# Performance work log

Measured on AMD Instinct MI355X. Metric: run time of the kernel, lower is better.

The kernel has to match this reference:

```python
import jax, jax.numpy as jnp
import numpy as np
import math

B, T, C = 1, 2048, 2048
N_HEAD = 32
N_QUERY_GROUPS = 8
HEAD_SIZE = 64
ROPE_N_ELEM = 16  # int(0.25 * 64)
Q_PER_KV = N_HEAD // N_QUERY_GROUPS  # 4
QKV_DIM = (N_HEAD + 2 * N_QUERY_GROUPS) * HEAD_SIZE  # 3072


def setup_inputs() -> dict:
    key = jax.random.key(0)
    ks = jax.random.split(key, 7)
    x = jax.random.normal(ks[0], (B, T, C), dtype=jnp.float32)
    # realistic rope tables
    inv_freq = 1.0 / (10000.0 ** (jnp.arange(0, ROPE_N_ELEM, 2, dtype=jnp.float32) / ROPE_N_ELEM))
    t = jnp.arange(T, dtype=jnp.float32)
    freqs = jnp.outer(t, inv_freq)                       # [T, rope/2]
    emb = jnp.concatenate([freqs, freqs], axis=-1)       # [T, rope]
    cos, sin = jnp.cos(emb), jnp.sin(emb)
    s = 0.02
    W_attn = jax.random.normal(ks[1], (QKV_DIM, C), dtype=jnp.float32) * s
    b_attn = jax.random.normal(ks[2], (QKV_DIM,), dtype=jnp.float32) * s
    W_proj = jax.random.normal(ks[3], (C, N_HEAD * HEAD_SIZE), dtype=jnp.float32) * s
    b_proj = jax.random.normal(ks[4], (C,), dtype=jnp.float32) * s
    return {"x": x, "cos": cos, "sin": sin, "W_attn": W_attn, "b_attn": b_attn,
            "W_proj": W_proj, "b_proj": b_proj}


def _apply_rope(t, cos, sin):
    # t: [B, H, T, rope]; cos/sin: [T, rope]
    half = t.shape[-1] // 2
    t1, t2 = t[..., :half], t[..., half:]
    rotated = jnp.concatenate([-t2, t1], axis=-1)
    return t * cos + rotated * sin


def reference(x, cos, sin, W_attn, b_attn, W_proj, b_proj):
    Bc, Tc, Cc = x.shape
    qkv = x @ W_attn.T + b_attn                                   # [B, T, 3072]
    qkv = qkv.reshape(Bc, Tc, N_QUERY_GROUPS, Q_PER_KV + 2, HEAD_SIZE)
    qkv = qkv.transpose(0, 2, 3, 1, 4)                            # [B, G, q_per_kv+2, T, hs]
    q = qkv[:, :, :Q_PER_KV]                                      # [B, G, q_per_kv, T, hs]
    k = qkv[:, :, Q_PER_KV:Q_PER_KV + 1]                          # [B, G, 1, T, hs]
    v = qkv[:, :, Q_PER_KV + 1:]
    # GQA expand (n_query_groups != n_head, prefill path)
    k = jnp.broadcast_to(k, (Bc, N_QUERY_GROUPS, Q_PER_KV, Tc, HEAD_SIZE))
    v = jnp.broadcast_to(v, (Bc, N_QUERY_GROUPS, Q_PER_KV, Tc, HEAD_SIZE))
    q = q.reshape(Bc, N_HEAD, Tc, HEAD_SIZE)
    k = k.reshape(Bc, N_HEAD, Tc, HEAD_SIZE)
    v = v.reshape(Bc, N_HEAD, Tc, HEAD_SIZE)
    # partial RoPE on first ROPE_N_ELEM dims
    q = jnp.concatenate([_apply_rope(q[..., :ROPE_N_ELEM], cos, sin), q[..., ROPE_N_ELEM:]], axis=-1)
    k = jnp.concatenate([_apply_rope(k[..., :ROPE_N_ELEM], cos, sin), k[..., ROPE_N_ELEM:]], axis=-1)
    # causal SDPA with scale 1/sqrt(head_size)
    scale = 1.0 / math.sqrt(HEAD_SIZE)
    scores = jnp.einsum('bhqd,bhkd->bhqk', q, k) * scale          # [B, H, T, T]
    causal = jnp.tril(jnp.ones((Tc, Tc), dtype=bool))
    scores = jnp.where(causal, scores, jnp.finfo(scores.dtype).min)
    attn = jax.nn.softmax(scores, axis=-1)
    y = jnp.einsum('bhqk,bhkd->bhqd', attn, v)                    # [B, H, T, hs]
    y = y.transpose(0, 2, 1, 3).reshape(Bc, Tc, N_HEAD * HEAD_SIZE)
    return y @ W_proj.T + b_proj
```

## Files before the change

kernel.cpp:

```cpp
#include <hip/hip_runtime.h>
#include <hip/hip_bf16.h>

using u16 = unsigned short;
typedef float f32x4 __attribute__((ext_vector_type(4)));
typedef __bf16 bf16x8 __attribute__((ext_vector_type(8)));

#define T_SEQ 2048
#define C_DIM 2048
#define QKV_DIM 3072
#define N_HEAD 32
#define N_GROUPS 8
#define HEAD_SIZE 64
#define ROPE_N 16
#define NEG_BIG (-1e30f)
#define LS 72

__device__ inline float bf2f(u16 u) {
    union { float f; unsigned v; } x; x.v = ((unsigned)u) << 16; return x.f;
}
__device__ inline u16 f2bf(float f) {
    __bf16 h = (__bf16)f;
    return *(u16*)&h;
}

__device__ __forceinline__ void gl_lds16(const u16* g, u16* l) {
    __builtin_amdgcn_global_load_lds(
        (const __attribute__((address_space(1))) unsigned int*)g,
        (__attribute__((address_space(3))) unsigned int*)l,
        16, 0, 0);
}

__global__ void detect_dtype(const u16* __restrict__ x, int* __restrict__ flag)
{
    __shared__ int s[256];
    int cnt = 0;
    for (int i = threadIdx.x; i < 8192; i += 256) {
        int e = (x[i] >> 7) & 0xFF;
        cnt += (e >= 0xC0);
    }
    s[threadIdx.x] = cnt;
    __syncthreads();
    if (threadIdx.x == 0) {
        int tot = 0;
        for (int i = 0; i < 256; i++) tot += s[i];
        flag[0] = (tot > 64) ? 1 : 0;
    }
}

struct ConvDesc {
    const void* src[7];
    u16*        dst[7];
    int         off8[8];
};

__global__ void convert_all(ConvDesc cd, const int* __restrict__ flag)
{
    int gid = blockIdx.x * blockDim.x + threadIdx.x;
    if (gid >= cd.off8[7]) return;
    int seg = 0;
#pragma unroll
    for (int s = 1; s < 7; s++) seg += (gid >= cd.off8[s]);
    int i = (gid - cd.off8[seg]) * 8;
    if (*flag) {
        const float4* s = (const float4*)((const float*)cd.src[seg] + i);
        float4 a = s[0], b = s[1];
        __attribute__((aligned(16))) u16 o[8] = {
            f2bf(a.x), f2bf(a.y), f2bf(a.z), f2bf(a.w),
            f2bf(b.x), f2bf(b.y), f2bf(b.z), f2bf(b.w) };
        *(int4*)(cd.dst[seg] + i) = *(const int4*)o;
    } else {
        *(int4*)(cd.dst[seg] + i) = *(const int4*)((const u16*)cd.src[seg] + i);
    }
}

__global__ __launch_bounds__(256) void gemm_qkv_rope(
    const u16* __restrict__ A, const u16* __restrict__ W,
    const u16* __restrict__ bias,
    const u16* __restrict__ ccos, const u16* __restrict__ csin,
    u16* __restrict__ Qout, u16* __restrict__ Kout, u16* __restrict__ Vtout)
{
    __shared__ __attribute__((aligned(16))) u16 lds_a[64 * 32];
    __shared__ __attribute__((aligned(16))) u16 lds_b[128 * 32];

    const int tid  = threadIdx.x;
    const int wave = tid >> 6;
    const int lane = tid & 63;
    const int quad = lane >> 4;
    const int l16  = lane & 15;
    const int bm = blockIdx.y * 64;
    const int bn = blockIdx.x * 128;
    const int K = C_DIM;

    f32x4 acc[4][2] = {};

    const int ra = tid >> 2,          ca = (tid & 3) * 8;
    const int rb0 = tid >> 2,         cb0 = (tid & 3) * 8;
    const int rb1 = (tid + 256) >> 2, cb1 = (tid & 3) * 8;

    for (int k0 = 0; k0 < K; k0 += 32) {
        __syncthreads();
        gl_lds16(A + (size_t)(bm + ra) * K + k0 + ca,  lds_a + tid * 8);
        gl_lds16(W + (size_t)(bn + rb0) * K + k0 + cb0, lds_b + tid * 8);
        gl_lds16(W + (size_t)(bn + rb1) * K + k0 + cb1, lds_b + (tid + 256) * 8);
        __syncthreads();

        bf16x8 afr[4], bfr[2];
#pragma unroll
        for (int i = 0; i < 4; i++)
            afr[i] = *(const bf16x8*)(lds_a + (i * 16 + l16) * 32 + quad * 8);
#pragma unroll
        for (int j = 0; j < 2; j++)
            bfr[j] = *(const bf16x8*)(lds_b + (wave * 32 + j * 16 + l16) * 32 + quad * 8);
#pragma unroll
        for (int i = 0; i < 4; i++)
#pragma unroll
            for (int j = 0; j < 2; j++)
                acc[i][j] = __builtin_amdgcn_mfma_f32_16x16x32_bf16(afr[i], bfr[j], acc[i][j], 0, 0, 0);
    }

#pragma unroll
    for (int j = 0; j < 2; j++) {
        const int colb = bn + wave * 32 + j * 16;
        const int col  = colb + l16;
        const int slot = (colb % 384) >> 6;
        const int g    = colb / 384;
        const int dbase = colb & 63;
        const int d    = dbase + l16;
        const float bv = bf2f(bias[col]);
        const bool rope = (dbase == 0) && (slot != 5);
#pragma unroll
        for (int i = 0; i < 4; i++) {
            const int trow = bm + i * 16 + quad * 4;
#pragma unroll
            for (int r = 0; r < 4; r++) {
                float v = acc[i][j][r] + bv;
                float outv = v;
                if (rope) {
                    float part = __shfl_xor(v, 8, 64);
                    float rot = (l16 < 8) ? -part : part;
                    float cc = bf2f(ccos[(trow + r) * ROPE_N + l16]);
                    float ss = bf2f(csin[(trow + r) * ROPE_N + l16]);
                    outv = v * cc + rot * ss;
                }
                const int t = trow + r;
                if (slot < 4) {
                    int hh = g * 4 + slot;
                    Qout[((size_t)hh * T_SEQ + t) * 64 + d] = f2bf(outv * 0.125f);
                } else if (slot == 4) {
                    Kout[((size_t)g * T_SEQ + t) * 64 + d] = f2bf(outv);
                } else {
                    Vtout[((size_t)g * 64 + d) * T_SEQ + t] = f2bf(outv);
                }
            }
        }
    }
}

__global__ __launch_bounds__(256) void gemm_bt(
    const u16* __restrict__ A, const u16* __restrict__ W,
    const u16* __restrict__ bias, u16* __restrict__ Cout,
    int M, int N, int K, const int* __restrict__ out_f32_flag)
{
    __shared__ __attribute__((aligned(16))) u16 lds_a[64 * 32];
    __shared__ __attribute__((aligned(16))) u16 lds_b[128 * 32];

    const int tid  = threadIdx.x;
    const int wave = tid >> 6;
    const int lane = tid & 63;
    const int quad = lane >> 4;
    const int l16  = lane & 15;
    const int bm = blockIdx.y * 64;
    const int bn = blockIdx.x * 128;

    f32x4 acc[4][2] = {};

    const int ra = tid >> 2,          ca = (tid & 3) * 8;
    const int rb1 = (tid + 256) >> 2;

    for (int k0 = 0; k0 < K; k0 += 32) {
        __syncthreads();
        gl_lds16(A + (size_t)(bm + ra) * K + k0 + ca,  lds_a + tid * 8);
        gl_lds16(W + (size_t)(bn + ra) * K + k0 + ca,  lds_b + tid * 8);
        gl_lds16(W + (size_t)(bn + rb1) * K + k0 + ca, lds_b + (tid + 256) * 8);
        __syncthreads();

        bf16x8 afr[4], bfr[2];
#pragma unroll
        for (int i = 0; i < 4; i++)
            afr[i] = *(const bf16x8*)(lds_a + (i * 16 + l16) * 32 + quad * 8);
#pragma unroll
        for (int j = 0; j < 2; j++)
            bfr[j] = *(const bf16x8*)(lds_b + (wave * 32 + j * 16 + l16) * 32 + quad * 8);
#pragma unroll
        for (int i = 0; i < 4; i++)
#pragma unroll
            for (int j = 0; j < 2; j++)
                acc[i][j] = __builtin_amdgcn_mfma_f32_16x16x32_bf16(afr[i], bfr[j], acc[i][j], 0, 0, 0);
    }

    const int of32 = out_f32_flag ? *out_f32_flag : 0;
#pragma unroll
    for (int i = 0; i < 4; i++) {
        int row = bm + i * 16 + quad * 4;
#pragma unroll
        for (int j = 0; j < 2; j++) {
            int col = bn + wave * 32 + j * 16 + l16;
            float bv = bf2f(bias[col]);
#pragma unroll
            for (int r = 0; r < 4; r++) {
                float v = acc[i][j][r] + bv;
                size_t idx = (size_t)(row + r) * N + col;
                if (of32) ((float*)Cout)[idx] = v;
                else      Cout[idx] = f2bf(v);
            }
        }
    }
}

__global__ __launch_bounds__(256) void flash_attn(
    const u16* __restrict__ Q, const u16* __restrict__ K,
    const u16* __restrict__ Vt, u16* __restrict__ Y)
{
    __shared__ __attribute__((aligned(16))) u16 lds_q[64 * LS];
    __shared__ __attribute__((aligned(16))) u16 lds_k[2][64 * LS];
    __shared__ __attribute__((aligned(16))) u16 lds_vt[2][64 * LS];
    __shared__ __attribute__((aligned(16))) u16 lds_p[4][16 * LS];

    const int h  = blockIdx.y;
    const int g  = h >> 2;
    const int tid  = threadIdx.x;
    const int wave = tid >> 6;
    const int lane = tid & 63;
    const int quad = lane >> 4;
    const int l16  = lane & 15;
    const int NQT = T_SEQ / 64;

    const u16* Qh = Q  + (size_t)h * T_SEQ * 64;
    const u16* Kg = K  + (size_t)g * T_SEQ * 64;
    const u16* Vg = Vt + (size_t)g * 64 * T_SEQ;

    const int srow = tid >> 3, scc = (tid & 7) * 8;

    int4 kr0, kr1, vr0, vr1;
    auto load_tile = [&](int k0) {
        kr0 = *(const int4*)(Kg + (size_t)(k0 + srow) * 64 + scc);
        kr1 = *(const int4*)(Kg + (size_t)(k0 + srow + 32) * 64 + scc);
        vr0 = *(const int4*)(Vg + (size_t)srow * T_SEQ + k0 + scc);
        vr1 = *(const int4*)(Vg + (size_t)(srow + 32) * T_SEQ + k0 + scc);
    };

    for (int pass = 0; pass < 2; pass++) {
        const int qt = pass ? (NQT - 1 - blockIdx.x) : blockIdx.x;
        const int q0 = qt * 64;

        __syncthreads();
        for (int s = tid; s < 512; s += 256) {
            int row = s >> 3, cc = (s & 7) * 8;
            *(int4*)(lds_q + row * LS + cc) =
                *(const int4*)(Qh + (size_t)(q0 + row) * 64 + cc);
        }
        __syncthreads();

        bf16x8 a_q[2];
#pragma unroll
        for (int ks = 0; ks < 2; ks++)
            a_q[ks] = *(const bf16x8*)(lds_q + (wave * 16 + l16) * LS + ks * 32 + quad * 8);

        float rs[4] = {0.f, 0.f, 0.f, 0.f};
        f32x4 o_acc[4] = {};

        load_tile(0);

        for (int kt = 0; kt <= qt; kt++) {
            const int p = kt & 1;
            *(int4*)(lds_k[p]  + srow * LS + scc)        = kr0;
            *(int4*)(lds_k[p]  + (srow + 32) * LS + scc) = kr1;
            *(int4*)(lds_vt[p] + srow * LS + scc)        = vr0;
            *(int4*)(lds_vt[p] + (srow + 32) * LS + scc) = vr1;
            __syncthreads();
            if (kt < qt) load_tile((kt + 1) * 64);

            f32x4 sc[4] = {};
#pragma unroll
            for (int ks = 0; ks < 2; ks++)
#pragma unroll
                for (int t = 0; t < 4; t++) {
                    bf16x8 bk = *(const bf16x8*)(lds_k[p] + (t * 16 + l16) * LS + ks * 32 + quad * 8);
                    sc[t] = __builtin_amdgcn_mfma_f32_16x16x32_bf16(a_q[ks], bk, sc[t], 0, 0, 0);
                }

            if (kt == qt) {
                const int row_g = q0 + wave * 16 + quad * 4;
                const int k0 = kt * 64;
#pragma unroll
                for (int t = 0; t < 4; t++) {
                    int col_g = k0 + t * 16 + l16;
#pragma unroll
                    for (int r = 0; r < 4; r++)
                        if (col_g > row_g + r) sc[t][r] = NEG_BIG;
                }
            }

#pragma unroll
            for (int t = 0; t < 4; t++) {
                int colo = t * 16 + l16;
#pragma unroll
                for (int r = 0; r < 4; r++) {
                    float pv = __expf(sc[t][r]);
                    rs[r] += pv;
                    lds_p[wave][(quad * 4 + r) * LS + colo] = f2bf(pv);
                }
            }
            __syncthreads();

#pragma unroll
            for (int ks = 0; ks < 2; ks++) {
                bf16x8 ap = *(const bf16x8*)(lds_p[wave] + l16 * LS + ks * 32 + quad * 8);
#pragma unroll
                for (int t = 0; t < 4; t++) {
                    bf16x8 bv = *(const bf16x8*)(lds_vt[p] + (t * 16 + l16) * LS + ks * 32 + quad * 8);
                    o_acc[t] = __builtin_amdgcn_mfma_f32_16x16x32_bf16(ap, bv, o_acc[t], 0, 0, 0);
                }
            }
        }

#pragma unroll
        for (int off = 1; off < 16; off <<= 1)
#pragma unroll
            for (int r = 0; r < 4; r++)
                rs[r] += __shfl_xor(rs[r], off, 64);

#pragma unroll
        for (int t = 0; t < 4; t++)
#pragma unroll
            for (int r = 0; r < 4; r++) {
                int row = q0 + wave * 16 + quad * 4 + r;
                int d   = t * 16 + l16;
                Y[(size_t)row * (N_HEAD * HEAD_SIZE) + h * 64 + d] = f2bf(o_acc[t][r] / rs[r]);
            }
    }
}

extern "C" void kernel_launch(void* const* d_in, const int* in_sizes, int n_in,
                              void* d_out, int out_size, void* d_ws, size_t ws_size,
                              hipStream_t stream)
{
    int* flag = (int*)d_ws;
    u16* base = (u16*)d_ws + 8;

    u16* cx   = base;
    u16* cWa  = cx  + (size_t)T_SEQ * C_DIM;
    u16* cba  = cWa + (size_t)QKV_DIM * C_DIM;
    u16* cWp  = cba + QKV_DIM;
    u16* cbp  = cWp + (size_t)C_DIM * C_DIM;
    u16* ccos = cbp + C_DIM;
    u16* csin = ccos + (size_t)T_SEQ * ROPE_N;
    u16* Qb   = csin + (size_t)T_SEQ * ROPE_N;
    u16* Kb   = Qb + (size_t)N_HEAD * T_SEQ * HEAD_SIZE;
    u16* Vtb  = Kb + (size_t)N_GROUPS * T_SEQ * HEAD_SIZE;
    u16* Yb   = Vtb + (size_t)N_GROUPS * T_SEQ * HEAD_SIZE;

    dim3 blk(256);

    detect_dtype<<<1, blk, 0, stream>>>((const u16*)d_in[0], flag);

    ConvDesc cd;
    const int sizes[7] = { T_SEQ * C_DIM, T_SEQ * ROPE_N, T_SEQ * ROPE_N,
                           QKV_DIM * C_DIM, QKV_DIM, C_DIM * C_DIM, C_DIM };
    u16* dsts[7] = { cx, ccos, csin, cWa, cba, cWp, cbp };
    int acc8 = 0;
    for (int i = 0; i < 7; i++) {
        cd.src[i] = d_in[i];
        cd.dst[i] = dsts[i];
        cd.off8[i] = acc8;
        acc8 += sizes[i] / 8;
    }
    cd.off8[7] = acc8;
    convert_all<<<dim3((acc8 + 255) / 256), blk, 0, stream>>>(cd, flag);

    gemm_qkv_rope<<<dim3(QKV_DIM / 128, T_SEQ / 64), blk, 0, stream>>>(
        cx, cWa, cba, ccos, csin, Qb, Kb, Vtb);
    flash_attn<<<dim3(T_SEQ / 128, N_HEAD), blk, 0, stream>>>(Qb, Kb, Vtb, Yb);
    gemm_bt<<<dim3(C_DIM / 128, T_SEQ / 64), blk, 0, stream>>>(
        Yb, cWp, cbp, (u16*)d_out, T_SEQ, C_DIM, N_HEAD * HEAD_SIZE, flag);
}
```

Before: 275.2 us.

## Fuse fp32-to-bf16 conversion of x and weights into GEMM tile loads

```diff
diff --git a/kernel.cpp b/kernel.cpp
--- a/kernel.cpp
+++ b/kernel.cpp
@@ -14,6 +14,7 @@
 #define ROPE_N 16
 #define NEG_BIG (-1e30f)
 #define LS 72
+#define GS 40
 
 __device__ inline float bf2f(u16 u) {
     union { float f; unsigned v; } x; x.v = ((unsigned)u) << 16; return x.f;
@@ -22,12 +23,13 @@
     __bf16 h = (__bf16)f;
     return *(u16*)&h;
 }
-
-__device__ __forceinline__ void gl_lds16(const u16* g, u16* l) {
-    __builtin_amdgcn_global_load_lds(
-        (const __attribute__((address_space(1))) unsigned int*)g,
-        (__attribute__((address_space(3))) unsigned int*)l,
-        16, 0, 0);
+__device__ inline int4 cvt8(int4 lo, int4 hi) {
+    const float* fa = (const float*)&lo;
+    const float* fb = (const float*)&hi;
+    __attribute__((aligned(16))) u16 o[8] = {
+        f2bf(fa[0]), f2bf(fa[1]), f2bf(fa[2]), f2bf(fa[3]),
+        f2bf(fb[0]), f2bf(fb[1]), f2bf(fb[2]), f2bf(fb[3]) };
+    return *(const int4*)o;
 }
 
 __global__ void detect_dtype(const u16* __restrict__ x, int* __restrict__ flag)
@@ -48,39 +50,36 @@
 }
 
 struct ConvDesc {
-    const void* src[7];
-    u16*        dst[7];
-    int         off8[8];
+    const void* src[4];
+    u16*        dst[4];
+    int         off8[5];
 };
 
-__global__ void convert_all(ConvDesc cd, const int* __restrict__ flag)
+__global__ void convert_small(ConvDesc cd, const int* __restrict__ flag)
 {
     int gid = blockIdx.x * blockDim.x + threadIdx.x;
-    if (gid >= cd.off8[7]) return;
+    if (gid >= cd.off8[4]) return;
     int seg = 0;
 #pragma unroll
-    for (int s = 1; s < 7; s++) seg += (gid >= cd.off8[s]);
+    for (int s = 1; s < 4; s++) seg += (gid >= cd.off8[s]);
     int i = (gid - cd.off8[seg]) * 8;
     if (*flag) {
         const float4* s = (const float4*)((const float*)cd.src[seg] + i);
-        float4 a = s[0], b = s[1];
-        __attribute__((aligned(16))) u16 o[8] = {
-            f2bf(a.x), f2bf(a.y), f2bf(a.z), f2bf(a.w),
-            f2bf(b.x), f2bf(b.y), f2bf(b.z), f2bf(b.w) };
-        *(int4*)(cd.dst[seg] + i) = *(const int4*)o;
+        *(int4*)(cd.dst[seg] + i) = cvt8(*(const int4*)&s[0], *(const int4*)&s[1]);
     } else {
         *(int4*)(cd.dst[seg] + i) = *(const int4*)((const u16*)cd.src[seg] + i);
     }
 }
 
 __global__ __launch_bounds__(256) void gemm_qkv_rope(
-    const u16* __restrict__ A, const u16* __restrict__ W,
+    const void* __restrict__ A, const void* __restrict__ W,
     const u16* __restrict__ bias,
     const u16* __restrict__ ccos, const u16* __restrict__ csin,
-    u16* __restrict__ Qout, u16* __restrict__ Kout, u16* __restrict__ Vtout)
-{
-    __shared__ __attribute__((aligned(16))) u16 lds_a[64 * 32];
-    __shared__ __attribute__((aligned(16))) u16 lds_b[128 * 32];
+    u16* __restrict__ Qout, u16* __restrict__ Kout, u16* __restrict__ Vtout,
+    const int* __restrict__ flag)
+{
+    __shared__ __attribute__((aligned(16))) u16 lds_a[2][64 * GS];
+    __shared__ __attribute__((aligned(16))) u16 lds_b[2][128 * GS];
 
     const int tid  = threadIdx.x;
     const int wave = tid >> 6;
@@ -90,27 +89,51 @@
     const int bm = blockIdx.y * 64;
     const int bn = blockIdx.x * 128;
     const int K = C_DIM;
+    const int fl = *flag;
 
     f32x4 acc[4][2] = {};
 
-    const int ra = tid >> 2,          ca = (tid & 3) * 8;
-    const int rb0 = tid >> 2,         cb0 = (tid & 3) * 8;
-    const int rb1 = (tid + 256) >> 2, cb1 = (tid & 3) * 8;
-
-    for (int k0 = 0; k0 < K; k0 += 32) {
+    const int ra = tid >> 2, ca = (tid & 3) * 8;
+    const int rb1 = ra + 64;
+
+    int4 ap[2], bp0[2], bp1[2];
+    auto load_tile = [&](int k0) {
+        size_t ea  = (size_t)(bm + ra) * K + k0 + ca;
+        size_t eb0 = (size_t)(bn + ra) * K + k0 + ca;
+        size_t eb1 = (size_t)(bn + rb1) * K + k0 + ca;
+        if (fl) {
+            const float* Af = (const float*)A; const float* Wf = (const float*)W;
+            ap[0]  = *(const int4*)(Af + ea);  ap[1]  = *(const int4*)(Af + ea + 4);
+            bp0[0] = *(const int4*)(Wf + eb0); bp0[1] = *(const int4*)(Wf + eb0 + 4);
+            bp1[0] = *(const int4*)(Wf + eb1); bp1[1] = *(const int4*)(Wf + eb1 + 4);
+        } else {
+            const u16* Ab = (const u16*)A; const u16* Wb = (const u16*)W;
+            ap[0]  = *(const int4*)(Ab + ea);
+            bp0[0] = *(const int4*)(Wb + eb0);
+            bp1[0] = *(const int4*)(Wb + eb1);
+        }
+    };
+
+    load_tile(0);
+    const int nsteps = K / 32;
+    for (int kt = 0; kt < nsteps; kt++) {
+        const int p = kt & 1;
+        int4 av  = fl ? cvt8(ap[0], ap[1])  : ap[0];
+        int4 bv0 = fl ? cvt8(bp0[0], bp0[1]) : bp0[0];
+        int4 bv1 = fl ? cvt8(bp1[0], bp1[1]) : bp1[0];
+        *(int4*)(lds_a[p] + ra * GS + ca)  = av;
+        *(int4*)(lds_b[p] + ra * GS + ca)  = bv0;
+        *(int4*)(lds_b[p] + rb1 * GS + ca) = bv1;
         __syncthreads();
-        gl_lds16(A + (size_t)(bm + ra) * K + k0 + ca,  lds_a + tid * 8);
-        gl_lds16(W + (size_t)(bn + rb0) * K + k0 + cb0, lds_b + tid * 8);
-        gl_lds16(W + (size_t)(bn + rb1) * K + k0 + cb1, lds_b + (tid + 256) * 8);
-        __syncthreads();
+        if (kt + 1 < nsteps) load_tile((kt + 1) * 32);
 
         bf16x8 afr[4], bfr[2];
 #pragma unroll
         for (int i = 0; i < 4; i++)
-            afr[i] = *(const bf16x8*)(lds_a + (i * 16 + l16) * 32 + quad * 8);
+            afr[i] = *(const bf16x8*)(lds_a[p] + (i * 16 + l16) * GS + quad * 8);
 #pragma unroll
         for (int j = 0; j < 2; j++)
-            bfr[j] = *(const bf16x8*)(lds_b + (wave * 32 + j * 16 + l16) * 32 + quad * 8);
+            bfr[j] = *(const bf16x8*)(lds_b[p] + (wave * 32 + j * 16 + l16) * GS + quad * 8);
 #pragma unroll
         for (int i = 0; i < 4; i++)
 #pragma unroll
@@ -157,12 +180,12 @@
 }
 
 __global__ __launch_bounds__(256) void gemm_bt(
-    const u16* __restrict__ A, const u16* __restrict__ W,
+    const u16* __restrict__ A, const void* __restrict__ W,
     const u16* __restrict__ bias, u16* __restrict__ Cout,
-    int M, int N, int K, const int* __restrict__ out_f32_flag)
-{
-    __shared__ __attribute__((aligned(16))) u16 lds_a[64 * 32];
-    __shared__ __attribute__((aligned(16))) u16 lds_b[128 * 32];
+    int M, int N, int K, const int* __restrict__ flag)
+{
+    __shared__ __attribute__((aligned(16))) u16 lds_a[2][64 * GS];
+    __shared__ __attribute__((aligned(16))) u16 lds_b[2][128 * GS];
 
     const int tid  = threadIdx.x;
     const int wave = tid >> 6;
@@ -171,26 +194,49 @@
     const int l16  = lane & 15;
     const int bm = blockIdx.y * 64;
     const int bn = blockIdx.x * 128;
+    const int fl = *flag;
 
     f32x4 acc[4][2] = {};
 
-    const int ra = tid >> 2,          ca = (tid & 3) * 8;
-    const int rb1 = (tid + 256) >> 2;
-
-    for (int k0 = 0; k0 < K; k0 += 32) {
+    const int ra = tid >> 2, ca = (tid & 3) * 8;
+    const int rb1 = ra + 64;
+
+    int4 ap, bp0[2], bp1[2];
+    auto load_tile = [&](int k0) {
+        size_t ea  = (size_t)(bm + ra) * K + k0 + ca;
+        size_t eb0 = (size_t)(bn + ra) * K + k0 + ca;
+        size_t eb1 = (size_t)(bn + rb1) * K + k0 + ca;
+        ap = *(const int4*)(A + ea);
+        if (fl) {
+            const float* Wf = (const float*)W;
+            bp0[0] = *(const int4*)(Wf + eb0); bp0[1] = *(const int4*)(Wf + eb0 + 4);
+            bp1[0] = *(const int4*)(Wf + eb1); bp1[1] = *(const int4*)(Wf + eb1 + 4);
+        } else {
+            const u16* Wb = (const u16*)W;
+            bp0[0] = *(const int4*)(Wb + eb0);
+            bp1[0] = *(const int4*)(Wb + eb1);
+        }
+    };
+
+    load_tile(0);
+    const int nsteps = K / 32;
+    for (int kt = 0; kt < nsteps; kt++) {
+        const int p = kt & 1;
+        int4 bv0 = fl ? cvt8(bp0[0], bp0[1]) : bp0[0];
+        int4 bv1 = fl ? cvt8(bp1[0], bp1[1]) : bp1[0];
+        *(int4*)(lds_a[p] + ra * GS + ca)  = ap;
+        *(int4*)(lds_b[p] + ra * GS + ca)  = bv0;
+        *(int4*)(lds_b[p] + rb1 * GS + ca) = bv1;
         __syncthreads();
-        gl_lds16(A + (size_t)(bm + ra) * K + k0 + ca,  lds_a + tid * 8);
-        gl_lds16(W + (size_t)(bn + ra) * K + k0 + ca,  lds_b + tid * 8);
-        gl_lds16(W + (size_t)(bn + rb1) * K + k0 + ca, lds_b + (tid + 256) * 8);
-        __syncthreads();
+        if (kt + 1 < nsteps) load_tile((kt + 1) * 32);
 
         bf16x8 afr[4], bfr[2];
 #pragma unroll
         for (int i = 0; i < 4; i++)
-            afr[i] = *(const bf16x8*)(lds_a + (i * 16 + l16) * 32 + quad * 8);
+            afr[i] = *(const bf16x8*)(lds_a[p] + (i * 16 + l16) * GS + quad * 8);
 #pragma unroll
         for (int j = 0; j < 2; j++)
-            bfr[j] = *(const bf16x8*)(lds_b + (wave * 32 + j * 16 + l16) * 32 + quad * 8);
+            bfr[j] = *(const bf16x8*)(lds_b[p] + (wave * 32 + j * 16 + l16) * GS + quad * 8);
 #pragma unroll
         for (int i = 0; i < 4; i++)
 #pragma unroll
@@ -198,7 +244,6 @@
                 acc[i][j] = __builtin_amdgcn_mfma_f32_16x16x32_bf16(afr[i], bfr[j], acc[i][j], 0, 0, 0);
     }
 
-    const int of32 = out_f32_flag ? *out_f32_flag : 0;
 #pragma unroll
     for (int i = 0; i < 4; i++) {
         int row = bm + i * 16 + quad * 4;
@@ -210,8 +255,8 @@
             for (int r = 0; r < 4; r++) {
                 float v = acc[i][j][r] + bv;
                 size_t idx = (size_t)(row + r) * N + col;
-                if (of32) ((float*)Cout)[idx] = v;
-                else      Cout[idx] = f2bf(v);
+                if (fl) ((float*)Cout)[idx] = v;
+                else    Cout[idx] = f2bf(v);
             }
         }
     }
@@ -315,11 +360,11 @@
 
 #pragma unroll
             for (int ks = 0; ks < 2; ks++) {
-                bf16x8 ap = *(const bf16x8*)(lds_p[wave] + l16 * LS + ks * 32 + quad * 8);
+                bf16x8 apf = *(const bf16x8*)(lds_p[wave] + l16 * LS + ks * 32 + quad * 8);
 #pragma unroll
                 for (int t = 0; t < 4; t++) {
-                    bf16x8 bv = *(const bf16x8*)(lds_vt[p] + (t * 16 + l16) * LS + ks * 32 + quad * 8);
-                    o_acc[t] = __builtin_amdgcn_mfma_f32_16x16x32_bf16(ap, bv, o_acc[t], 0, 0, 0);
+                    bf16x8 bvf = *(const bf16x8*)(lds_vt[p] + (t * 16 + l16) * LS + ks * 32 + quad * 8);
+                    o_acc[t] = __builtin_amdgcn_mfma_f32_16x16x32_bf16(apf, bvf, o_acc[t], 0, 0, 0);
                 }
             }
         }
@@ -348,11 +393,8 @@
     int* flag = (int*)d_ws;
     u16* base = (u16*)d_ws + 8;
 
-    u16* cx   = base;
-    u16* cWa  = cx  + (size_t)T_SEQ * C_DIM;
-    u16* cba  = cWa + (size_t)QKV_DIM * C_DIM;
-    u16* cWp  = cba + QKV_DIM;
-    u16* cbp  = cWp + (size_t)C_DIM * C_DIM;
+    u16* cba  = base;
+    u16* cbp  = cba + QKV_DIM;
     u16* ccos = cbp + C_DIM;
     u16* csin = ccos + (size_t)T_SEQ * ROPE_N;
     u16* Qb   = csin + (size_t)T_SEQ * ROPE_N;
@@ -365,22 +407,22 @@
     detect_dtype<<<1, blk, 0, stream>>>((const u16*)d_in[0], flag);
 
     ConvDesc cd;
-    const int sizes[7] = { T_SEQ * C_DIM, T_SEQ * ROPE_N, T_SEQ * ROPE_N,
-                           QKV_DIM * C_DIM, QKV_DIM, C_DIM * C_DIM, C_DIM };
-    u16* dsts[7] = { cx, ccos, csin, cWa, cba, cWp, cbp };
+    const int sizes[4] = { T_SEQ * ROPE_N, T_SEQ * ROPE_N, QKV_DIM, C_DIM };
+    const void* srcs[4] = { d_in[1], d_in[2], d_in[4], d_in[6] };
+    u16* dsts[4] = { ccos, csin, cba, cbp };
     int acc8 = 0;
-    for (int i = 0; i < 7; i++) {
-        cd.src[i] = d_in[i];
+    for (int i = 0; i < 4; i++) {
+        cd.src[i] = srcs[i];
         cd.dst[i] = dsts[i];
         cd.off8[i] = acc8;
         acc8 += sizes[i] / 8;
     }
-    cd.off8[7] = acc8;
-    convert_all<<<dim3((acc8 + 255) / 256), blk, 0, stream>>>(cd, flag);
+    cd.off8[4] = acc8;
+    convert_small<<<dim3((acc8 + 255) / 256), blk, 0, stream>>>(cd, flag);
 
     gemm_qkv_rope<<<dim3(QKV_DIM / 128, T_SEQ / 64), blk, 0, stream>>>(
-        cx, cWa, cba, ccos, csin, Qb, Kb, Vtb);
+        d_in[0], d_in[3], cba, ccos, csin, Qb, Kb, Vtb, flag);
     flash_attn<<<dim3(T_SEQ / 128, N_HEAD), blk, 0, stream>>>(Qb, Kb, Vtb, Yb);
     gemm_bt<<<dim3(C_DIM / 128, T_SEQ / 64), blk, 0, stream>>>(
-        Yb, cWp, cbp, (u16*)d_out, T_SEQ, C_DIM, N_HEAD * HEAD_SIZE, flag);
-}
+        Yb, d_in[5], cbp, (u16*)d_out, T_SEQ, C_DIM, N_HEAD * HEAD_SIZE, flag);
+}
```

Result: slower. 292.1 us (+6.1%).

## Double-buffer GEMM tiles via register prefetch with padded LDS stride

Applied to the files above, without the earlier changes.

```diff
diff --git a/kernel.cpp b/kernel.cpp
--- a/kernel.cpp
+++ b/kernel.cpp
@@ -14,6 +14,7 @@
 #define ROPE_N 16
 #define NEG_BIG (-1e30f)
 #define LS 72
+#define GS 40
 
 __device__ inline float bf2f(u16 u) {
     union { float f; unsigned v; } x; x.v = ((unsigned)u) << 16; return x.f;
@@ -22,12 +23,13 @@
     __bf16 h = (__bf16)f;
     return *(u16*)&h;
 }
-
-__device__ __forceinline__ void gl_lds16(const u16* g, u16* l) {
-    __builtin_amdgcn_global_load_lds(
-        (const __attribute__((address_space(1))) unsigned int*)g,
-        (__attribute__((address_space(3))) unsigned int*)l,
-        16, 0, 0);
+__device__ inline int4 cvt8(int4 lo, int4 hi) {
+    const float* fa = (const float*)&lo;
+    const float* fb = (const float*)&hi;
+    __attribute__((aligned(16))) u16 o[8] = {
+        f2bf(fa[0]), f2bf(fa[1]), f2bf(fa[2]), f2bf(fa[3]),
+        f2bf(fb[0]), f2bf(fb[1]), f2bf(fb[2]), f2bf(fb[3]) };
+    return *(const int4*)o;
 }
 
 __global__ void detect_dtype(const u16* __restrict__ x, int* __restrict__ flag)
@@ -63,11 +65,7 @@
     int i = (gid - cd.off8[seg]) * 8;
     if (*flag) {
         const float4* s = (const float4*)((const float*)cd.src[seg] + i);
-        float4 a = s[0], b = s[1];
-        __attribute__((aligned(16))) u16 o[8] = {
-            f2bf(a.x), f2bf(a.y), f2bf(a.z), f2bf(a.w),
-            f2bf(b.x), f2bf(b.y), f2bf(b.z), f2bf(b.w) };
-        *(int4*)(cd.dst[seg] + i) = *(const int4*)o;
+        *(int4*)(cd.dst[seg] + i) = cvt8(*(const int4*)&s[0], *(const int4*)&s[1]);
     } else {
         *(int4*)(cd.dst[seg] + i) = *(const int4*)((const u16*)cd.src[seg] + i);
     }
@@ -79,8 +77,8 @@
     const u16* __restrict__ ccos, const u16* __restrict__ csin,
     u16* __restrict__ Qout, u16* __restrict__ Kout, u16* __restrict__ Vtout)
 {
-    __shared__ __attribute__((aligned(16))) u16 lds_a[64 * 32];
-    __shared__ __attribute__((aligned(16))) u16 lds_b[128 * 32];
+    __shared__ __attribute__((aligned(16))) u16 lds_a[2][64 * GS];
+    __shared__ __attribute__((aligned(16))) u16 lds_b[2][128 * GS];
 
     const int tid  = threadIdx.x;
     const int wave = tid >> 6;
@@ -93,24 +91,33 @@
 
     f32x4 acc[4][2] = {};
 
-    const int ra = tid >> 2,          ca = (tid & 3) * 8;
-    const int rb0 = tid >> 2,         cb0 = (tid & 3) * 8;
-    const int rb1 = (tid + 256) >> 2, cb1 = (tid & 3) * 8;
-
-    for (int k0 = 0; k0 < K; k0 += 32) {
+    const int ra = tid >> 2, ca = (tid & 3) * 8;
+    const int rb1 = ra + 64;
+
+    int4 ap, bp0, bp1;
+    auto load_tile = [&](int k0) {
+        ap  = *(const int4*)(A + (size_t)(bm + ra) * K + k0 + ca);
+        bp0 = *(const int4*)(W + (size_t)(bn + ra) * K + k0 + ca);
+        bp1 = *(const int4*)(W + (size_t)(bn + rb1) * K + k0 + ca);
+    };
+
+    load_tile(0);
+    const int nsteps = K / 32;
+    for (int kt = 0; kt < nsteps; kt++) {
+        const int p = kt & 1;
+        *(int4*)(lds_a[p] + ra * GS + ca)  = ap;
+        *(int4*)(lds_b[p] + ra * GS + ca)  = bp0;
+        *(int4*)(lds_b[p] + rb1 * GS + ca) = bp1;
         __syncthreads();
-        gl_lds16(A + (size_t)(bm + ra) * K + k0 + ca,  lds_a + tid * 8);
-        gl_lds16(W + (size_t)(bn + rb0) * K + k0 + cb0, lds_b + tid * 8);
-        gl_lds16(W + (size_t)(bn + rb1) * K + k0 + cb1, lds_b + (tid + 256) * 8);
-        __syncthreads();
+        if (kt + 1 < nsteps) load_tile((kt + 1) * 32);
 
         bf16x8 afr[4], bfr[2];
 #pragma unroll
         for (int i = 0; i < 4; i++)
-            afr[i] = *(const bf16x8*)(lds_a + (i * 16 + l16) * 32 + quad * 8);
+            afr[i] = *(const bf16x8*)(lds_a[p] + (i * 16 + l16) * GS + quad * 8);
 #pragma unroll
         for (int j = 0; j < 2; j++)
-            bfr[j] = *(const bf16x8*)(lds_b + (wave * 32 + j * 16 + l16) * 32 + quad * 8);
+            bfr[j] = *(const bf16x8*)(lds_b[p] + (wave * 32 + j * 16 + l16) * GS + quad * 8);
 #pragma unroll
         for (int i = 0; i < 4; i++)
 #pragma unroll
@@ -159,10 +166,10 @@
 __global__ __launch_bounds__(256) void gemm_bt(
     const u16* __restrict__ A, const u16* __restrict__ W,
     const u16* __restrict__ bias, u16* __restrict__ Cout,
-    int M, int N, int K, const int* __restrict__ out_f32_flag)
-{
-    __shared__ __attribute__((aligned(16))) u16 lds_a[64 * 32];
-    __shared__ __attribute__((aligned(16))) u16 lds_b[128 * 32];
+    int M, int N, int K, const int* __restrict__ flag)
+{
+    __shared__ __attribute__((aligned(16))) u16 lds_a[2][64 * GS];
+    __shared__ __attribute__((aligned(16))) u16 lds_b[2][128 * GS];
 
     const int tid  = threadIdx.x;
     const int wave = tid >> 6;
@@ -171,26 +178,37 @@
     const int l16  = lane & 15;
     const int bm = blockIdx.y * 64;
     const int bn = blockIdx.x * 128;
+    const int fl = *flag;
 
     f32x4 acc[4][2] = {};
 
-    const int ra = tid >> 2,          ca = (tid & 3) * 8;
-    const int rb1 = (tid + 256) >> 2;
-
-    for (int k0 = 0; k0 < K; k0 += 32) {
+    const int ra = tid >> 2, ca = (tid & 3) * 8;
+    const int rb1 = ra + 64;
+
+    int4 ap, bp0, bp1;
+    auto load_tile = [&](int k0) {
+        ap  = *(const int4*)(A + (size_t)(bm + ra) * K + k0 + ca);
+        bp0 = *(const int4*)(W + (size_t)(bn + ra) * K + k0 + ca);
+        bp1 = *(const int4*)(W + (size_t)(bn + rb1) * K + k0 + ca);
+    };
+
+    load_tile(0);
+    const int nsteps = K / 32;
+    for (int kt = 0; kt < nsteps; kt++) {
+        const int p = kt & 1;
+        *(int4*)(lds_a[p] + ra * GS + ca)  = ap;
+        *(int4*)(lds_b[p] + ra * GS + ca)  = bp0;
+        *(int4*)(lds_b[p] + rb1 * GS + ca) = bp1;
         __syncthreads();
-        gl_lds16(A + (size_t)(bm + ra) * K + k0 + ca,  lds_a + tid * 8);
-        gl_lds16(W + (size_t)(bn + ra) * K + k0 + ca,  lds_b + tid * 8);
-        gl_lds16(W + (size_t)(bn + rb1) * K + k0 + ca, lds_b + (tid + 256) * 8);
-        __syncthreads();
+        if (kt + 1 < nsteps) load_tile((kt + 1) * 32);
 
         bf16x8 afr[4], bfr[2];
 #pragma unroll
         for (int i = 0; i < 4; i++)
-            afr[i] = *(const bf16x8*)(lds_a + (i * 16 + l16) * 32 + quad * 8);
+            afr[i] = *(const bf16x8*)(lds_a[p] + (i * 16 + l16) * GS + quad * 8);
 #pragma unroll
         for (int j = 0; j < 2; j++)
-            bfr[j] = *(const bf16x8*)(lds_b + (wave * 32 + j * 16 + l16) * 32 + quad * 8);
+            bfr[j] = *(const bf16x8*)(lds_b[p] + (wave * 32 + j * 16 + l16) * GS + quad * 8);
 #pragma unroll
         for (int i = 0; i < 4; i++)
 #pragma unroll
@@ -198,7 +216,6 @@
                 acc[i][j] = __builtin_amdgcn_mfma_f32_16x16x32_bf16(afr[i], bfr[j], acc[i][j], 0, 0, 0);
     }
 
-    const int of32 = out_f32_flag ? *out_f32_flag : 0;
 #pragma unroll
     for (int i = 0; i < 4; i++) {
         int row = bm + i * 16 + quad * 4;
@@ -210,8 +227,8 @@
             for (int r = 0; r < 4; r++) {
                 float v = acc[i][j][r] + bv;
                 size_t idx = (size_t)(row + r) * N + col;
-                if (of32) ((float*)Cout)[idx] = v;
-                else      Cout[idx] = f2bf(v);
+                if (fl) ((float*)Cout)[idx] = v;
+                else    Cout[idx] = f2bf(v);
             }
         }
     }
@@ -315,11 +332,11 @@
 
 #pragma unroll
             for (int ks = 0; ks < 2; ks++) {
-                bf16x8 ap = *(const bf16x8*)(lds_p[wave] + l16 * LS + ks * 32 + quad * 8);
+                bf16x8 apf = *(const bf16x8*)(lds_p[wave] + l16 * LS + ks * 32 + quad * 8);
 #pragma unroll
                 for (int t = 0; t < 4; t++) {
-                    bf16x8 bv = *(const bf16x8*)(lds_vt[p] + (t * 16 + l16) * LS + ks * 32 + quad * 8);
-                    o_acc[t] = __builtin_amdgcn_mfma_f32_16x16x32_bf16(ap, bv, o_acc[t], 0, 0, 0);
+                    bf16x8 bvf = *(const bf16x8*)(lds_vt[p] + (t * 16 + l16) * LS + ks * 32 + quad * 8);
+                    o_acc[t] = __builtin_amdgcn_mfma_f32_16x16x32_bf16(apf, bvf, o_acc[t], 0, 0, 0);
                 }
             }
         }
```

Measured after the change: 270.9 us. No clear change (-1.6%).

## Enlarge QKV GEMM tile to 128x128 and give flash attention 128-row query tiles

Applied to the files above, without the earlier changes.

```diff
diff --git a/kernel.cpp b/kernel.cpp
--- a/kernel.cpp
+++ b/kernel.cpp
@@ -22,6 +22,14 @@
     __bf16 h = (__bf16)f;
     return *(u16*)&h;
 }
+__device__ inline int4 cvt8(int4 lo, int4 hi) {
+    const float* fa = (const float*)&lo;
+    const float* fb = (const float*)&hi;
+    __attribute__((aligned(16))) u16 o[8] = {
+        f2bf(fa[0]), f2bf(fa[1]), f2bf(fa[2]), f2bf(fa[3]),
+        f2bf(fb[0]), f2bf(fb[1]), f2bf(fb[2]), f2bf(fb[3]) };
+    return *(const int4*)o;
+}
 
 __device__ __forceinline__ void gl_lds16(const u16* g, u16* l) {
     __builtin_amdgcn_global_load_lds(
@@ -63,11 +71,7 @@
     int i = (gid - cd.off8[seg]) * 8;
     if (*flag) {
         const float4* s = (const float4*)((const float*)cd.src[seg] + i);
-        float4 a = s[0], b = s[1];
-        __attribute__((aligned(16))) u16 o[8] = {
-            f2bf(a.x), f2bf(a.y), f2bf(a.z), f2bf(a.w),
-            f2bf(b.x), f2bf(b.y), f2bf(b.z), f2bf(b.w) };
-        *(int4*)(cd.dst[seg] + i) = *(const int4*)o;
+        *(int4*)(cd.dst[seg] + i) = cvt8(*(const int4*)&s[0], *(const int4*)&s[1]);
     } else {
         *(int4*)(cd.dst[seg] + i) = *(const int4*)((const u16*)cd.src[seg] + i);
     }
@@ -79,7 +83,7 @@
     const u16* __restrict__ ccos, const u16* __restrict__ csin,
     u16* __restrict__ Qout, u16* __restrict__ Kout, u16* __restrict__ Vtout)
 {
-    __shared__ __attribute__((aligned(16))) u16 lds_a[64 * 32];
+    __shared__ __attribute__((aligned(16))) u16 lds_a[128 * 32];
     __shared__ __attribute__((aligned(16))) u16 lds_b[128 * 32];
 
     const int tid  = threadIdx.x;
@@ -87,40 +91,42 @@
     const int lane = tid & 63;
     const int quad = lane >> 4;
     const int l16  = lane & 15;
-    const int bm = blockIdx.y * 64;
+    const int wr = wave >> 1, wc = wave & 1;
+    const int bm = blockIdx.y * 128;
     const int bn = blockIdx.x * 128;
     const int K = C_DIM;
 
-    f32x4 acc[4][2] = {};
-
-    const int ra = tid >> 2,          ca = (tid & 3) * 8;
-    const int rb0 = tid >> 2,         cb0 = (tid & 3) * 8;
-    const int rb1 = (tid + 256) >> 2, cb1 = (tid & 3) * 8;
+    f32x4 acc[4][4] = {};
+
+    const int s0 = tid, s1 = tid + 256;
+    const int r0 = s0 >> 2, c0 = (s0 & 3) * 8;
+    const int r1 = s1 >> 2, c1 = (s1 & 3) * 8;
 
     for (int k0 = 0; k0 < K; k0 += 32) {
         __syncthreads();
-        gl_lds16(A + (size_t)(bm + ra) * K + k0 + ca,  lds_a + tid * 8);
-        gl_lds16(W + (size_t)(bn + rb0) * K + k0 + cb0, lds_b + tid * 8);
-        gl_lds16(W + (size_t)(bn + rb1) * K + k0 + cb1, lds_b + (tid + 256) * 8);
-        __syncthreads();
-
-        bf16x8 afr[4], bfr[2];
+        gl_lds16(A + (size_t)(bm + r0) * K + k0 + c0, lds_a + s0 * 8);
+        gl_lds16(A + (size_t)(bm + r1) * K + k0 + c1, lds_a + s1 * 8);
+        gl_lds16(W + (size_t)(bn + r0) * K + k0 + c0, lds_b + s0 * 8);
+        gl_lds16(W + (size_t)(bn + r1) * K + k0 + c1, lds_b + s1 * 8);
+        __syncthreads();
+
+        bf16x8 afr[4], bfr[4];
 #pragma unroll
         for (int i = 0; i < 4; i++)
-            afr[i] = *(const bf16x8*)(lds_a + (i * 16 + l16) * 32 + quad * 8);
-#pragma unroll
-        for (int j = 0; j < 2; j++)
-            bfr[j] = *(const bf16x8*)(lds_b + (wave * 32 + j * 16 + l16) * 32 + quad * 8);
+            afr[i] = *(const bf16x8*)(lds_a + (wr * 64 + i * 16 + l16) * 32 + quad * 8);
+#pragma unroll
+        for (int j = 0; j < 4; j++)
+            bfr[j] = *(const bf16x8*)(lds_b + (wc * 64 + j * 16 + l16) * 32 + quad * 8);
 #pragma unroll
         for (int i = 0; i < 4; i++)
 #pragma unroll
-            for (int j = 0; j < 2; j++)
+            for (int j = 0; j < 4; j++)
                 acc[i][j] = __builtin_amdgcn_mfma_f32_16x16x32_bf16(afr[i], bfr[j], acc[i][j], 0, 0, 0);
     }
 
 #pragma unroll
-    for (int j = 0; j < 2; j++) {
-        const int colb = bn + wave * 32 + j * 16;
+    for (int j = 0; j < 4; j++) {
+        const int colb = bn + wc * 64 + j * 16;
         const int col  = colb + l16;
         const int slot = (colb % 384) >> 6;
         const int g    = colb / 384;
@@ -130,7 +136,7 @@
         const bool rope = (dbase == 0) && (slot != 5);
 #pragma unroll
         for (int i = 0; i < 4; i++) {
-            const int trow = bm + i * 16 + quad * 4;
+            const int trow = bm + wr * 64 + i * 16 + quad * 4;
 #pragma unroll
             for (int r = 0; r < 4; r++) {
                 float v = acc[i][j][r] + bv;
@@ -159,7 +165,7 @@
 __global__ __launch_bounds__(256) void gemm_bt(
     const u16* __restrict__ A, const u16* __restrict__ W,
     const u16* __restrict__ bias, u16* __restrict__ Cout,
-    int M, int N, int K, const int* __restrict__ out_f32_flag)
+    int M, int N, int K, const int* __restrict__ flag)
 {
     __shared__ __attribute__((aligned(16))) u16 lds_a[64 * 32];
     __shared__ __attribute__((aligned(16))) u16 lds_b[128 * 32];
@@ -171,10 +177,11 @@
     const int l16  = lane & 15;
     const int bm = blockIdx.y * 64;
     const int bn = blockIdx.x * 128;
+    const int fl = *flag;
 
     f32x4 acc[4][2] = {};
 
-    const int ra = tid >> 2,          ca = (tid & 3) * 8;
+    const int ra = tid >> 2, ca = (tid & 3) * 8;
     const int rb1 = (tid + 256) >> 2;
 
     for (int k0 = 0; k0 < K; k0 += 32) {
@@ -198,7 +205,6 @@
                 acc[i][j] = __builtin_amdgcn_mfma_f32_16x16x32_bf16(afr[i], bfr[j], acc[i][j], 0, 0, 0);
     }
 
-    const int of32 = out_f32_flag ? *out_f32_flag : 0;
 #pragma unroll
     for (int i = 0; i < 4; i++) {
         int row = bm + i * 16 + quad * 4;
@@ -210,8 +216,8 @@
             for (int r = 0; r < 4; r++) {
                 float v = acc[i][j][r] + bv;
                 size_t idx = (size_t)(row + r) * N + col;
-                if (of32) ((float*)Cout)[idx] = v;
-                else      Cout[idx] = f2bf(v);
+                if (fl) ((float*)Cout)[idx] = v;
+                else    Cout[idx] = f2bf(v);
             }
         }
     }
@@ -221,26 +227,43 @@
     const u16* __restrict__ Q, const u16* __restrict__ K,
     const u16* __restrict__ Vt, u16* __restrict__ Y)
 {
-    __shared__ __attribute__((aligned(16))) u16 lds_q[64 * LS];
+    __shared__ __attribute__((aligned(16))) u16 lds_q[128 * LS];
     __shared__ __attribute__((aligned(16))) u16 lds_k[2][64 * LS];
     __shared__ __attribute__((aligned(16))) u16 lds_vt[2][64 * LS];
-    __shared__ __attribute__((aligned(16))) u16 lds_p[4][16 * LS];
+    __shared__ __attribute__((aligned(16))) u16 lds_p[4][32 * LS];
 
     const int h  = blockIdx.y;
     const int g  = h >> 2;
+    const int qt = blockIdx.x;
+    const int q0 = qt * 128;
     const int tid  = threadIdx.x;
     const int wave = tid >> 6;
     const int lane = tid & 63;
     const int quad = lane >> 4;
     const int l16  = lane & 15;
-    const int NQT = T_SEQ / 64;
 
     const u16* Qh = Q  + (size_t)h * T_SEQ * 64;
     const u16* Kg = K  + (size_t)g * T_SEQ * 64;
     const u16* Vg = Vt + (size_t)g * 64 * T_SEQ;
 
+    for (int s = tid; s < 1024; s += 256) {
+        int row = s >> 3, cc = (s & 7) * 8;
+        *(int4*)(lds_q + row * LS + cc) =
+            *(const int4*)(Qh + (size_t)(q0 + row) * 64 + cc);
+    }
+    __syncthreads();
+
+    bf16x8 a_q[2][2];
+#pragma unroll
+    for (int s = 0; s < 2; s++)
+#pragma unroll
+        for (int ks = 0; ks < 2; ks++)
+            a_q[s][ks] = *(const bf16x8*)(lds_q + (wave * 32 + s * 16 + l16) * LS + ks * 32 + quad * 8);
+
+    float rs[2][4] = {};
+    f32x4 o_acc[2][4] = {};
+
     const int srow = tid >> 3, scc = (tid & 7) * 8;
-
     int4 kr0, kr1, vr0, vr1;
     auto load_tile = [&](int k0) {
         kr0 = *(const int4*)(Kg + (size_t)(k0 + srow) * 64 + scc);
@@ -249,96 +272,95 @@
         vr1 = *(const int4*)(Vg + (size_t)(srow + 32) * T_SEQ + k0 + scc);
     };
 
-    for (int pass = 0; pass < 2; pass++) {
-        const int qt = pass ? (NQT - 1 - blockIdx.x) : blockIdx.x;
-        const int q0 = qt * 64;
-
-        __syncthreads();
-        for (int s = tid; s < 512; s += 256) {
-            int row = s >> 3, cc = (s & 7) * 8;
-            *(int4*)(lds_q + row * LS + cc) =
-                *(const int4*)(Qh + (size_t)(q0 + row) * 64 + cc);
+    const int n_kt = 2 * qt + 2;
+    load_tile(0);
+
+    for (int kt = 0; kt < n_kt; kt++) {
+        const int p = kt & 1;
+        const int k0 = kt * 64;
+        *(int4*)(lds_k[p]  + srow * LS + scc)        = kr0;
+        *(int4*)(lds_k[p]  + (srow + 32) * LS + scc) = kr1;
+        *(int4*)(lds_vt[p] + srow * LS + scc)        = vr0;
+        *(int4*)(lds_vt[p] + (srow + 32) * LS + scc) = vr1;
+        __syncthreads();
+        if (kt + 1 < n_kt) load_tile((kt + 1) * 64);
+
+        f32x4 sc[2][4] = {};
+#pragma unroll
+        for (int ks = 0; ks < 2; ks++) {
+            bf16x8 bk[4];
+#pragma unroll
+            for (int t = 0; t < 4; t++)
+                bk[t] = *(const bf16x8*)(lds_k[p] + (t * 16 + l16) * LS + ks * 32 + quad * 8);
+#pragma unroll
+            for (int s = 0; s < 2; s++)
+#pragma unroll
+                for (int t = 0; t < 4; t++)
+                    sc[s][t] = __builtin_amdgcn_mfma_f32_16x16x32_bf16(a_q[s][ks], bk[t], sc[s][t], 0, 0, 0);
         }
-        __syncthreads();
-
-        bf16x8 a_q[2];
-#pragma unroll
-        for (int ks = 0; ks < 2; ks++)
-            a_q[ks] = *(const bf16x8*)(lds_q + (wave * 16 + l16) * LS + ks * 32 + quad * 8);
-
-        float rs[4] = {0.f, 0.f, 0.f, 0.f};
-        f32x4 o_acc[4] = {};
-
-        load_tile(0);
-
-        for (int kt = 0; kt <= qt; kt++) {
-            const int p = kt & 1;
-            *(int4*)(lds_k[p]  + srow * LS + scc)        = kr0;
-            *(int4*)(lds_k[p]  + (srow + 32) * LS + scc) = kr1;
-            *(int4*)(lds_vt[p] + srow * LS + scc)        = vr0;
-            *(int4*)(lds_vt[p] + (srow + 32) * LS + scc) = vr1;
-            __syncthreads();
-            if (kt < qt) load_tile((kt + 1) * 64);
-
-            f32x4 sc[4] = {};
-#pragma unroll
-            for (int ks = 0; ks < 2; ks++)
-#pragma unroll
-                for (int t = 0; t < 4; t++) {
-                    bf16x8 bk = *(const bf16x8*)(lds_k[p] + (t * 16 + l16) * LS + ks * 32 + quad * 8);
-                    sc[t] = __builtin_amdgcn_mfma_f32_16x16x32_bf16(a_q[ks], bk, sc[t], 0, 0, 0);
-                }
-
-            if (kt == qt) {
-                const int row_g = q0 + wave * 16 + quad * 4;
-                const int k0 = kt * 64;
+
+#pragma unroll
+        for (int s = 0; s < 2; s++) {
+            const int rsb = q0 + wave * 32 + s * 16 + quad * 4;
+            if (k0 + 63 > rsb) {
 #pragma unroll
                 for (int t = 0; t < 4; t++) {
                     int col_g = k0 + t * 16 + l16;
 #pragma unroll
                     for (int r = 0; r < 4; r++)
-                        if (col_g > row_g + r) sc[t][r] = NEG_BIG;
+                        if (col_g > rsb + r) sc[s][t][r] = NEG_BIG;
                 }
             }
-
+        }
+
+#pragma unroll
+        for (int s = 0; s < 2; s++)
 #pragma unroll
             for (int t = 0; t < 4; t++) {
                 int colo = t * 16 + l16;
 #pragma unroll
                 for (int r = 0; r < 4; r++) {
-                    float pv = __expf(sc[t][r]);
-                    rs[r] += pv;
-                    lds_p[wave][(quad * 4 + r) * LS + colo] = f2bf(pv);
+                    float pv = __expf(sc[s][t][r]);
+                    rs[s][r] += pv;
+                    lds_p[wave][(s * 16 + quad * 4 + r) * LS + colo] = f2bf(pv);
                 }
             }
-            __syncthreads();
-
-#pragma unroll
-            for (int ks = 0; ks < 2; ks++) {
-                bf16x8 ap = *(const bf16x8*)(lds_p[wave] + l16 * LS + ks * 32 + quad * 8);
-#pragma unroll
-                for (int t = 0; t < 4; t++) {
-                    bf16x8 bv = *(const bf16x8*)(lds_vt[p] + (t * 16 + l16) * LS + ks * 32 + quad * 8);
-                    o_acc[t] = __builtin_amdgcn_mfma_f32_16x16x32_bf16(ap, bv, o_acc[t], 0, 0, 0);
-                }
+        __syncthreads();
+
+#pragma unroll
+        for (int ks = 0; ks < 2; ks++) {
+            bf16x8 bv[4];
+#pragma unroll
+            for (int t = 0; t < 4; t++)
+                bv[t] = *(const bf16x8*)(lds_vt[p] + (t * 16 + l16) * LS + ks * 32 + quad * 8);
+#pragma unroll
+            for (int s = 0; s < 2; s++) {
+                bf16x8 apf = *(const bf16x8*)(lds_p[wave] + (s * 16 + l16) * LS + ks * 32 + quad * 8);
+#pragma unroll
+                for (int t = 0; t < 4; t++)
+                    o_acc[s][t] = __builtin_amdgcn_mfma_f32_16x16x32_bf16(apf, bv[t], o_acc[s][t], 0, 0, 0);
             }
         }
-
-#pragma unroll
-        for (int off = 1; off < 16; off <<= 1)
+    }
+
+#pragma unroll
+    for (int off = 1; off < 16; off <<= 1)
+#pragma unroll
+        for (int s = 0; s < 2; s++)
 #pragma unroll
             for (int r = 0; r < 4; r++)
-                rs[r] += __shfl_xor(rs[r], off, 64);
-
+                rs[s][r] += __shfl_xor(rs[s][r], off, 64);
+
+#pragma unroll
+    for (int s = 0; s < 2; s++)
 #pragma unroll
         for (int t = 0; t < 4; t++)
 #pragma unroll
             for (int r = 0; r < 4; r++) {
-                int row = q0 + wave * 16 + quad * 4 + r;
+                int row = q0 + wave * 32 + s * 16 + quad * 4 + r;
                 int d   = t * 16 + l16;
-                Y[(size_t)row * (N_HEAD * HEAD_SIZE) + h * 64 + d] = f2bf(o_acc[t][r] / rs[r]);
-            }
-    }
+                Y[(size_t)row * (N_HEAD * HEAD_SIZE) + h * 64 + d] = f2bf(o_acc[s][t][r] / rs[s][r]);
+            }
 }
 
 extern "C" void kernel_launch(void* const* d_in, const int* in_sizes, int n_in,
@@ -378,7 +400,7 @@
     cd.off8[7] = acc8;
     convert_all<<<dim3((acc8 + 255) / 256), blk, 0, stream>>>(cd, flag);
 
-    gemm_qkv_rope<<<dim3(QKV_DIM / 128, T_SEQ / 64), blk, 0, stream>>>(
+    gemm_qkv_rope<<<dim3(QKV_DIM / 128, T_SEQ / 128), blk, 0, stream>>>(
         cx, cWa, cba, ccos, csin, Qb, Kb, Vtb);
     flash_attn<<<dim3(T_SEQ / 128, N_HEAD), blk, 0, stream>>>(Qb, Kb, Vtb, Yb);
     gemm_bt<<<dim3(C_DIM / 128, T_SEQ / 64), blk, 0, stream>>>(
```

New measurement: 296.4 us. 7.7% more time.
